# Kernel optimization log

Measured on AMD Instinct MI355X. Metric: run time of the kernel, lower is better.

Reference implementation:

```python
import jax, jax.numpy as jnp
import numpy as np

N_NODES = 50000
N_EDGES = 800000
N_REL = 8
OUT_CH = 64      # latent dim of z
HID = 128        # hidden_channels
IN_CH = 128      # reconstructed feature dim
NEG_SLOPE = 0.2


def rgat_conv(x, src, dst, edge_type, weight, q, k, bias, num_nodes):
    """PyG RGATConv, heads=1, dim=1, additive-self-attention, across-relation.
    x: [N, in]; weight: [R, in, out]; q,k: [out, 1]; bias: [out]."""
    # per-relation transform of all nodes, then per-edge gather (same math as
    # per-edge bmm with weight[edge_type], avoids [E, in, out] intermediate)
    x_all = jnp.einsum('ni,rio->nro', x, weight)          # [N, R, out]
    x_j = x_all[src, edge_type]                            # [E, out]
    x_i = x_all[dst, edge_type]                            # [E, out]
    alpha = (x_i @ q + x_j @ k)[:, 0]                      # [E]
    alpha = jax.nn.leaky_relu(alpha, NEG_SLOPE)
    # scatter-softmax over destination neighborhoods
    m = jax.ops.segment_max(alpha, dst, num_segments=num_nodes)
    m = jnp.where(jnp.isfinite(m), m, 0.0)                 # empty segments -> 0
    ex = jnp.exp(alpha - m[dst])
    denom = jax.ops.segment_sum(ex, dst, num_segments=num_nodes)
    a = ex / (denom[dst] + 1e-16)                          # [E]
    out = jax.ops.segment_sum(a[:, None] * x_j, dst, num_segments=num_nodes)
    return out + bias


def setup_inputs() -> dict:
    key = jax.random.key(0)
    ks = jax.random.split(key, 12)
    z = jax.random.normal(ks[0], (N_NODES, OUT_CH), dtype=jnp.float32)
    edge_index = jax.random.randint(ks[1], (2, N_EDGES), 0, N_NODES, dtype=jnp.int32)
    edge_type = jax.random.randint(ks[2], (N_EDGES,), 0, N_REL, dtype=jnp.int32)

    def glorot(k_, shape):
        fan = shape[-2] + shape[-1]
        return jax.random.normal(k_, shape, dtype=jnp.float32) * jnp.sqrt(2.0 / fan)

    return {
        'z': z,
        'lin_w': glorot(ks[3], (HID, OUT_CH)),
        'lin_b': jnp.zeros((HID,), dtype=jnp.float32),
        'w1': glorot(ks[4], (N_REL, HID, HID)),
        'q1': glorot(ks[5], (HID, 1)),
        'k1': glorot(ks[6], (HID, 1)),
        'b1': jnp.zeros((HID,), dtype=jnp.float32),
        'w2': glorot(ks[7], (N_REL, HID, IN_CH)),
        'q2': glorot(ks[8], (IN_CH, 1)),
        'k2': glorot(ks[9], (IN_CH, 1)),
        'b2': jnp.zeros((IN_CH,), dtype=jnp.float32),
        'edge_index': edge_index,
        'edge_type': edge_type,
    }


def reference(z, lin_w, lin_b, w1, q1, k1, b1, w2, q2, k2, b2, edge_index, edge_type):
    num_nodes = z.shape[0]
    src, dst = edge_index[0], edge_index[1]
    h = z @ lin_w.T + lin_b                                 # nn.Linear
    h = jax.nn.relu(rgat_conv(h, src, dst, edge_type, w1, q1, k1, b1, num_nodes))
    # dropout is identity in eval mode
    recon_x = rgat_conv(h, src, dst, edge_type, w2, q2, k2, b2, num_nodes)
    return recon_x
```

## Files before the change

kernel.cpp:

```cpp
#include <hip/hip_runtime.h>
#include <hip/hip_bf16.h>
#include <cstdint>
#include <cstddef>

#define N_NODES 50000
#define N_EDGES 800000
#define NSEG    (N_NODES * 8)

using frag_t = __attribute__((ext_vector_type(8))) short;
using f32x4  = __attribute__((ext_vector_type(4))) float;

typedef const __attribute__((address_space(1))) void* gptr_t;
typedef __attribute__((address_space(3))) void* lptr_t;

__device__ __forceinline__ short f2bf(float x) {
    __hip_bfloat16 h = __float2bfloat16(x);
    return *reinterpret_cast<short*>(&h);
}
__device__ __forceinline__ float bf2f(unsigned int u) {
    union { unsigned int i; float f; } v;
    v.i = u << 16;
    return v.f;
}
__device__ __forceinline__ unsigned int packbf2(float lo, float hi) {
    unsigned int a = (unsigned short)f2bf(lo);
    unsigned int b = (unsigned short)f2bf(hi);
    return a | (b << 16);
}


__global__ void hist_kernel(const int* __restrict__ dst, const int* __restrict__ et,
                            int* __restrict__ deg8, int E) {
    int e = blockIdx.x * 256 + threadIdx.x;
    if (e < E) atomicAdd(&deg8[dst[e] * 8 + et[e]], 1);
}

__global__ __launch_bounds__(256) void scan_part(const int* __restrict__ deg8,
                                                 int* __restrict__ part, int M) {
    __shared__ int red[256];
    int t = threadIdx.x;
    int idx = blockIdx.x * 1024 + t * 4;
    int s = 0;
    if (idx + 3 < M) {
        int4 d = *(const int4*)(deg8 + idx);
        s = d.x + d.y + d.z + d.w;
    } else {
        for (int c = 0; c < 4; c++) if (idx + c < M) s += deg8[idx + c];
    }
    red[t] = s;
    __syncthreads();
    #pragma unroll
    for (int off = 128; off; off >>= 1) {
        if (t < off) red[t] += red[t + off];
        __syncthreads();
    }
    if (t == 0) part[blockIdx.x] = red[0];
}

__global__ __launch_bounds__(512) void scan_mid(int* __restrict__ part, int nparts,
                                                int* __restrict__ rowp, int M) {
    __shared__ int buf[512];
    int t = threadIdx.x;
    int own = (t < nparts) ? part[t] : 0;
    buf[t] = own;
    __syncthreads();
    for (int off = 1; off < 512; off <<= 1) {
        int v = buf[t];
        int u = (t >= off) ? buf[t - off] : 0;
        __syncthreads();
        buf[t] = v + u;
        __syncthreads();
    }
    if (t < nparts) part[t] = buf[t] - own;
    if (t == 511) rowp[M] = buf[511];
}

__global__ __launch_bounds__(256) void scan_fix(const int* __restrict__ deg8,
                                                const int* __restrict__ part,
                                                int* __restrict__ rowp,
                                                int* __restrict__ cursor, int M) {
    __shared__ int wsum[4];
    int t = threadIdx.x, lane = t & 63, w = t >> 6;
    int idx = blockIdx.x * 1024 + t * 4;
    int v0 = 0, v1 = 0, v2 = 0, v3 = 0;
    if (idx + 3 < M) {
        int4 d = *(const int4*)(deg8 + idx);
        v0 = d.x; v1 = d.y; v2 = d.z; v3 = d.w;
    } else {
        if (idx     < M) v0 = deg8[idx];
        if (idx + 1 < M) v1 = deg8[idx + 1];
        if (idx + 2 < M) v2 = deg8[idx + 2];
        if (idx + 3 < M) v3 = deg8[idx + 3];
    }
    int tsum = v0 + v1 + v2 + v3;
    int sc = tsum;
    #pragma unroll
    for (int off = 1; off < 64; off <<= 1) {
        int u = __shfl_up(sc, off, 64);
        if (lane >= off) sc += u;
    }
    if (lane == 63) wsum[w] = sc;
    __syncthreads();
    int woff = 0;
    for (int i = 0; i < w; i++) woff += wsum[i];
    int excl = part[blockIdx.x] + woff + sc - tsum;
    if (idx     < M) { rowp[idx]     = excl; cursor[idx]     = excl; } excl += v0;
    if (idx + 1 < M) { rowp[idx + 1] = excl; cursor[idx + 1] = excl; } excl += v1;
    if (idx + 2 < M) { rowp[idx + 2] = excl; cursor[idx + 2] = excl; } excl += v2;
    if (idx + 3 < M) { rowp[idx + 3] = excl; cursor[idx + 3] = excl; }
}

__global__ void fill_kernel(const int* __restrict__ src, const int* __restrict__ dst,
                            const int* __restrict__ et, int* __restrict__ cursor,
                            int* __restrict__ sorted, int E) {
    int e = blockIdx.x * 256 + threadIdx.x;
    if (e < E) {
        int pos = atomicAdd(&cursor[dst[e] * 8 + et[e]], 1);
        sorted[pos] = src[e] | (et[e] << 16);
    }
}


__global__ __launch_bounds__(256) void gemm_lin(const float* __restrict__ A,
                                                const float* __restrict__ B,
                                                const float* __restrict__ bias,
                                                unsigned short* __restrict__ hb, int N) {
    const int Kdim = 64;
    __shared__ float As[32][64];
    __shared__ float Bs[32][128];
    int t = threadIdx.x;
    int n0 = blockIdx.x * 64;
    int rg = t >> 4, cg = t & 15;
    int an = t >> 2, ak = (t & 3) * 8;
    float acc[4][8] = {};

    for (int k0 = 0; k0 < Kdim; k0 += 32) {
        int gn = n0 + an;
        if (gn < N) {
            const float* ap = A + (size_t)gn * Kdim + k0 + ak;
            float4 v0 = *(const float4*)ap;
            float4 v1 = *(const float4*)(ap + 4);
            As[ak + 0][an] = v0.x; As[ak + 1][an] = v0.y;
            As[ak + 2][an] = v0.z; As[ak + 3][an] = v0.w;
            As[ak + 4][an] = v1.x; As[ak + 5][an] = v1.y;
            As[ak + 6][an] = v1.z; As[ak + 7][an] = v1.w;
        } else {
            #pragma unroll
            for (int c = 0; c < 8; c++) As[ak + c][an] = 0.f;
        }
        {
            int o = t >> 1, kh = (t & 1) * 16;
            const float* bp = B + (size_t)o * Kdim + k0 + kh;
            #pragma unroll
            for (int j = 0; j < 4; j++) {
                float4 v = ((const float4*)bp)[j];
                Bs[kh + j * 4 + 0][o] = v.x;
                Bs[kh + j * 4 + 1][o] = v.y;
                Bs[kh + j * 4 + 2][o] = v.z;
                Bs[kh + j * 4 + 3][o] = v.w;
            }
        }
        __syncthreads();
        #pragma unroll
        for (int k = 0; k < 32; k++) {
            float a[4], b[8];
            *(float4*)&a[0] = *(const float4*)&As[k][rg * 4];
            *(float4*)&b[0] = *(const float4*)&Bs[k][cg * 8];
            *(float4*)&b[4] = *(const float4*)&Bs[k][cg * 8 + 4];
            #pragma unroll
            for (int i = 0; i < 4; i++)
                #pragma unroll
                for (int j = 0; j < 8; j++)
                    acc[i][j] = fmaf(a[i], b[j], acc[i][j]);
        }
        __syncthreads();
    }
    #pragma unroll
    for (int i = 0; i < 4; i++) {
        int gn = n0 + rg * 4 + i;
        if (gn < N) {
            unsigned short us[8];
            #pragma unroll
            for (int j = 0; j < 8; j++)
                us[j] = (unsigned short)f2bf(acc[i][j] + bias[cg * 8 + j]);
            *(int4*)(hb + (size_t)gn * 128 + cg * 8) = *(int4*)&us[0];
        }
    }
}


__global__ void wprep_kernel(const float* __restrict__ W, const float* __restrict__ q,
                             const float* __restrict__ k, short* __restrict__ Bf,
                             float* __restrict__ wq, float* __restrict__ wk) {
    int g = blockIdx.x * 256 + threadIdx.x;
    if (g < 131072) {
        int kk = g >> 7, o = g & 127;
        float v = W[(size_t)kk * 128 + o];
        Bf[(((size_t)(kk >> 3) * 128) + o) * 8 + (kk & 7)] = f2bf(v);
        return;
    }
    int h = g - 131072;
    if (h < 2048) {
        int which = h >> 10;
        int r = (h >> 7) & 7;
        int i = h & 127;
        const float* vec = which ? k : q;
        const float* wrow = W + ((size_t)r * 128 + i) * 128;
        float acc = 0.f;
        #pragma unroll 4
        for (int o = 0; o < 128; o++) acc = fmaf(wrow[o], vec[o], acc);
        (which ? wk : wq)[r * 128 + i] = acc;
    }
}


__global__ __launch_bounds__(256) void qk_table_kernel(const unsigned short* __restrict__ xb,
                                                       const float* __restrict__ wq,
                                                       const float* __restrict__ wk,
                                                       float* __restrict__ Q,
                                                       float* __restrict__ K, int N) {
    int n = blockIdx.x * 256 + threadIdx.x;
    if (n >= N) return;
    const uint2* row = (const uint2*)(xb + (size_t)n * 128);
    float aq[8] = {}, ak[8] = {};
    for (int i = 0; i < 32; i++) {
        uint2 d = row[i];
        float x0 = bf2f(d.x & 0xFFFFu);
        float x1 = bf2f(d.x >> 16);
        float x2 = bf2f(d.y & 0xFFFFu);
        float x3 = bf2f(d.y >> 16);
        int c = i * 4;
        #pragma unroll
        for (int r = 0; r < 8; r++) {
            const float* wqr = wq + r * 128 + c;
            const float* wkr = wk + r * 128 + c;
            aq[r] = fmaf(x0, wqr[0], fmaf(x1, wqr[1], fmaf(x2, wqr[2], fmaf(x3, wqr[3], aq[r]))));
            ak[r] = fmaf(x0, wkr[0], fmaf(x1, wkr[1], fmaf(x2, wkr[2], fmaf(x3, wkr[3], ak[r]))));
        }
    }
    float4* qp = (float4*)(Q + (size_t)n * 8);
    qp[0] = *(float4*)&aq[0];
    qp[1] = *(float4*)&aq[4];
    float4* kp = (float4*)(K + (size_t)n * 8);
    kp[0] = *(float4*)&ak[0];
    kp[1] = *(float4*)&ak[4];
}


__global__ __launch_bounds__(256) void agg_s_kernel(const unsigned short* __restrict__ hb,
                                                    const float* __restrict__ Q,
                                                    const float* __restrict__ Kt,
                                                    const int* __restrict__ rowp8,
                                                    const int* __restrict__ sorted,
                                                    short* __restrict__ s, int N) {
    int wv = threadIdx.x >> 6;
    int lane = threadIdx.x & 63;
    int n = blockIdx.x * 4 + wv;
    if (n >= N) return;
    int beg = rowp8[n * 8];
    int end = rowp8[n * 8 + 8];
    int deg = end - beg;
    unsigned int* spw = (unsigned int*)(s + (size_t)n * 1024);
    const unsigned int* hbu = (const unsigned int*)hb;

    if (deg == 0) {
        int4 z = {0, 0, 0, 0};
        int4* p = (int4*)spw;
        p[lane * 2]     = z;
        p[lane * 2 + 1] = z;
        return;
    }

    float2 acc = {0.f, 0.f};
    int rcur = 0;

    if (deg <= 64) {
        int pk = 0;
        float a = -INFINITY;
        if (lane < deg) {
            pk = sorted[beg + lane];
            int srcn = pk & 0xFFFF, etj = pk >> 16;
            a = Q[(size_t)n * 8 + etj] + Kt[(size_t)srcn * 8 + etj];
            a = (a > 0.f) ? a : 0.2f * a;
        }
        float m = a;
        #pragma unroll
        for (int off = 32; off; off >>= 1) m = fmaxf(m, __shfl_xor(m, off, 64));
        float e = (lane < deg) ? __expf(a - m) : 0.f;
        float sum = e;
        #pragma unroll
        for (int off = 32; off; off >>= 1) sum += __shfl_xor(sum, off, 64);
        float w = e / (sum + 1e-16f);

        int j = 0;
        for (; j + 8 <= deg; j += 8) {
            int pp[8]; float ww[8]; unsigned int dd[8];
            #pragma unroll
            for (int i = 0; i < 8; i++) {
                pp[i] = __shfl(pk, j + i, 64);
                ww[i] = __shfl(w,  j + i, 64);
            }
            #pragma unroll
            for (int i = 0; i < 8; i++)
                dd[i] = hbu[(size_t)(pp[i] & 0xFFFF) * 64 + lane];
            #pragma unroll
            for (int i = 0; i < 8; i++) {
                int e0 = pp[i] >> 16;
                while (rcur < e0) { spw[rcur * 64 + lane] = packbf2(acc.x, acc.y); acc.x = acc.y = 0.f; rcur++; }
                acc.x = fmaf(ww[i], bf2f(dd[i] & 0xFFFF), acc.x);
                acc.y = fmaf(ww[i], bf2f(dd[i] >> 16),    acc.y);
            }
        }
        for (; j < deg; j++) {
            int   p0 = __shfl(pk, j, 64);
            float w0 = __shfl(w, j, 64);
            unsigned int d0 = hbu[(size_t)(p0 & 0xFFFF) * 64 + lane];
            int e0 = p0 >> 16;
            while (rcur < e0) { spw[rcur * 64 + lane] = packbf2(acc.x, acc.y); acc.x = acc.y = 0.f; rcur++; }
            acc.x = fmaf(w0, bf2f(d0 & 0xFFFF), acc.x);
            acc.y = fmaf(w0, bf2f(d0 >> 16),    acc.y);
        }
        while (rcur < 8) { spw[rcur * 64 + lane] = packbf2(acc.x, acc.y); acc.x = acc.y = 0.f; rcur++; }
        return;
    }

    auto logit = [&](int j) -> float {
        int pk = sorted[beg + j];
        int srcn = pk & 0xFFFF, etj = pk >> 16;
        float a = Q[(size_t)n * 8 + etj] + Kt[(size_t)srcn * 8 + etj];
        return (a > 0.f) ? a : 0.2f * a;
    };
    float m = -INFINITY;
    for (int j = lane; j < deg; j += 64) m = fmaxf(m, logit(j));
    #pragma unroll
    for (int off = 32; off; off >>= 1) m = fmaxf(m, __shfl_xor(m, off, 64));
    float sum = 0.f;
    for (int j = lane; j < deg; j += 64) sum += __expf(logit(j) - m);
    #pragma unroll
    for (int off = 32; off; off >>= 1) sum += __shfl_xor(sum, off, 64);
    float inv = 1.f / (sum + 1e-16f);

    for (int j0 = 0; j0 < deg; j0 += 64) {
        int cnt = min(64, deg - j0);
        int pk = 0;
        float w = 0.f;
        if (lane < cnt) {
            pk = sorted[beg + j0 + lane];
            int srcn = pk & 0xFFFF, etj = pk >> 16;
            float a = Q[(size_t)n * 8 + etj] + Kt[(size_t)srcn * 8 + etj];
            a = (a > 0.f) ? a : 0.2f * a;
            w = __expf(a - m) * inv;
        }
        for (int j = 0; j < cnt; j++) {
            int   p0 = __shfl(pk, j, 64);
            float w0 = __shfl(w, j, 64);
            unsigned int d0 = hbu[(size_t)(p0 & 0xFFFF) * 64 + lane];
            int e0 = p0 >> 16;
            while (rcur < e0) { spw[rcur * 64 + lane] = packbf2(acc.x, acc.y); acc.x = acc.y = 0.f; rcur++; }
            acc.x = fmaf(w0, bf2f(d0 & 0xFFFF), acc.x);
            acc.y = fmaf(w0, bf2f(d0 >> 16),    acc.y);
        }
    }
    while (rcur < 8) { spw[rcur * 64 + lane] = packbf2(acc.x, acc.y); acc.x = acc.y = 0.f; rcur++; }
}


__global__ __launch_bounds__(256) void gemm_mfma(const short* __restrict__ s,
                                                 const short* __restrict__ Bf,
                                                 const float* __restrict__ bias,
                                                 float* __restrict__ Cout,
                                                 unsigned short* __restrict__ hbout,
                                                 int N, int relu) {
    __shared__ short As[4096];
    __shared__ short Bs[4096];
    int t = threadIdx.x;
    int w = t >> 6, lane = t & 63;
    int lhi = lane >> 4, llo = lane & 15;
    int n0 = blockIdx.x * 128;
    const char* sB = (const char*)s;
    const char* bB = (const char*)Bf;
    f32x4 acc[16] = {};

    for (int c = 0; c < 32; c++) {
        #pragma unroll
        for (int i = 0; i < 2; i++) {
            int row = i * 64 + lane;
            const void* gp = sB + (size_t)(n0 + row) * 2048 + c * 64 + w * 16;
            __builtin_amdgcn_global_load_lds(
                (gptr_t)gp, (lptr_t)((char*)As + w * 2048 + i * 1024), 16, 0, 0);
        }
        #pragma unroll
        for (int i = 0; i < 2; i++) {
            const void* gp = bB + (size_t)c * 8192 + w * 2048 + i * 1024 + lane * 16;
            __builtin_amdgcn_global_load_lds(
                (gptr_t)gp, (lptr_t)((char*)Bs + w * 2048 + i * 1024), 16, 0, 0);
        }
        __syncthreads();
        frag_t a0 = *(const frag_t*)(As + ((size_t)lhi * 128 + w * 32 + llo) * 8);
        frag_t a1 = *(const frag_t*)(As + ((size_t)lhi * 128 + w * 32 + llo + 16) * 8);
        #pragma unroll
        for (int ct = 0; ct < 8; ct++) {
            frag_t b = *(const frag_t*)(Bs + ((size_t)lhi * 128 + ct * 16 + llo) * 8);
            acc[ct]     = __builtin_amdgcn_mfma_f32_16x16x32_bf16(a0, b, acc[ct], 0, 0, 0);
            acc[8 + ct] = __builtin_amdgcn_mfma_f32_16x16x32_bf16(a1, b, acc[8 + ct], 0, 0, 0);
        }
        __syncthreads();
    }
    #pragma unroll
    for (int rt = 0; rt < 2; rt++) {
        #pragma unroll
        for (int ct = 0; ct < 8; ct++) {
            int col = ct * 16 + llo;
            float bv = bias[col];
            #pragma unroll
            for (int rg = 0; rg < 4; rg++) {
                int rown = n0 + w * 32 + rt * 16 + lhi * 4 + rg;
                if (rown < N) {
                    float v = acc[rt * 8 + ct][rg] + bv;
                    if (relu) v = fmaxf(v, 0.f);
                    if (Cout)  Cout[(size_t)rown * 128 + col] = v;
                    if (hbout) hbout[(size_t)rown * 128 + col] = (unsigned short)f2bf(v);
                }
            }
        }
    }
}


extern "C" void kernel_launch(void* const* d_in, const int* in_sizes, int n_in,
                              void* d_out, int out_size, void* d_ws, size_t ws_size,
                              hipStream_t stream) {
    const float* z     = (const float*)d_in[0];
    const float* lin_w = (const float*)d_in[1];
    const float* lin_b = (const float*)d_in[2];
    const float* w1    = (const float*)d_in[3];
    const float* q1    = (const float*)d_in[4];
    const float* k1    = (const float*)d_in[5];
    const float* b1    = (const float*)d_in[6];
    const float* w2    = (const float*)d_in[7];
    const float* q2    = (const float*)d_in[8];
    const float* k2    = (const float*)d_in[9];
    const float* b2    = (const float*)d_in[10];
    const int*   ei    = (const int*)d_in[11];
    const int*   et    = (const int*)d_in[12];
    float* out = (float*)d_out;

    char* ws = (char*)d_ws;
    size_t off = 0;
    auto alloc = [&](size_t bytes) -> void* {
        void* p = ws + off;
        off += (bytes + 255) & ~(size_t)255;
        return p;
    };
    short* s     = (short*)alloc((size_t)N_NODES * 1024 * 2);
    unsigned short* hb = (unsigned short*)alloc((size_t)N_NODES * 128 * 2);
    float* Q     = (float*)alloc((size_t)N_NODES * 8 * 4);
    float* K     = (float*)alloc((size_t)N_NODES * 8 * 4);
    int* sorted  = (int*)alloc((size_t)N_EDGES * 4);
    int* deg8    = (int*)alloc((size_t)NSEG * 4);
    int* rowp8   = (int*)alloc((size_t)(NSEG + 1) * 4);
    int* cursor8 = (int*)alloc((size_t)NSEG * 4);
    int* part    = (int*)alloc(1024 * 4);
    float* wq    = (float*)alloc(8 * 128 * 4);
    float* wk    = (float*)alloc(8 * 128 * 4);
    short* Bf    = (short*)alloc((size_t)1024 * 128 * 2);

    const int* src = ei;
    const int* dst = ei + N_EDGES;

    const int M = NSEG;
    const int nparts = (M + 1023) / 1024;

    hipMemsetAsync(deg8, 0, (size_t)M * 4, stream);
    hist_kernel<<<(N_EDGES + 255) / 256, 256, 0, stream>>>(dst, et, deg8, N_EDGES);
    scan_part<<<nparts, 256, 0, stream>>>(deg8, part, M);
    scan_mid<<<1, 512, 0, stream>>>(part, nparts, rowp8, M);
    scan_fix<<<nparts, 256, 0, stream>>>(deg8, part, rowp8, cursor8, M);
    fill_kernel<<<(N_EDGES + 255) / 256, 256, 0, stream>>>(src, dst, et, cursor8, sorted, N_EDGES);

    gemm_lin<<<(N_NODES + 63) / 64, 256, 0, stream>>>(z, lin_w, lin_b, hb, N_NODES);

    int mgrid = (N_NODES + 127) / 128;
    int agrid = (N_NODES + 3) / 4;
    int qgrid = (N_NODES + 255) / 256;
    int wgrid = (131072 + 2048) / 256;

    wprep_kernel<<<wgrid, 256, 0, stream>>>(w1, q1, k1, Bf, wq, wk);
    qk_table_kernel<<<qgrid, 256, 0, stream>>>(hb, wq, wk, Q, K, N_NODES);
    agg_s_kernel<<<agrid, 256, 0, stream>>>(hb, Q, K, rowp8, sorted, s, N_NODES);
    gemm_mfma<<<mgrid, 256, 0, stream>>>(s, Bf, b1, (float*)nullptr, hb, N_NODES, 1);

    wprep_kernel<<<wgrid, 256, 0, stream>>>(w2, q2, k2, Bf, wq, wk);
    qk_table_kernel<<<qgrid, 256, 0, stream>>>(hb, wq, wk, Q, K, N_NODES);
    agg_s_kernel<<<agrid, 256, 0, stream>>>(hb, Q, K, rowp8, sorted, s, N_NODES);
    gemm_mfma<<<mgrid, 256, 0, stream>>>(s, Bf, b2, out, (unsigned short*)nullptr, N_NODES, 0);
}
```

Before: 411.3 us.

## Fuse neighbor aggregation into MFMA GEMM with relation-major CSR layout

Edges are now bucketed relation-major (per relation, then per destination node), and attention weights are computed in a separate weight_kernel that writes per-edge alphas. A new fused kernel aggregates each relation's weighted neighbor features for a 64-node tile directly into shared memory, then runs that relation's MFMA GEMM slice. This avoids writing and re-reading the large N x 1024 bf16 intermediate s buffer. In exchange it adds an alpha buffer, a second hb buffer, eight serialized gather/GEMM phases per block with syncs, and smaller tiles.

```diff
diff --git a/kernel.cpp b/kernel.cpp
--- a/kernel.cpp
+++ b/kernel.cpp
@@ -30,22 +30,22 @@
 
 
 __global__ void hist_kernel(const int* __restrict__ dst, const int* __restrict__ et,
-                            int* __restrict__ deg8, int E) {
+                            int* __restrict__ deg2, int E) {
     int e = blockIdx.x * 256 + threadIdx.x;
-    if (e < E) atomicAdd(&deg8[dst[e] * 8 + et[e]], 1);
-}
-
-__global__ __launch_bounds__(256) void scan_part(const int* __restrict__ deg8,
+    if (e < E) atomicAdd(&deg2[et[e] * N_NODES + dst[e]], 1);
+}
+
+__global__ __launch_bounds__(256) void scan_part(const int* __restrict__ deg2,
                                                  int* __restrict__ part, int M) {
     __shared__ int red[256];
     int t = threadIdx.x;
     int idx = blockIdx.x * 1024 + t * 4;
     int s = 0;
     if (idx + 3 < M) {
-        int4 d = *(const int4*)(deg8 + idx);
+        int4 d = *(const int4*)(deg2 + idx);
         s = d.x + d.y + d.z + d.w;
     } else {
-        for (int c = 0; c < 4; c++) if (idx + c < M) s += deg8[idx + c];
+        for (int c = 0; c < 4; c++) if (idx + c < M) s += deg2[idx + c];
     }
     red[t] = s;
     __syncthreads();
@@ -75,7 +75,7 @@
     if (t == 511) rowp[M] = buf[511];
 }
 
-__global__ __launch_bounds__(256) void scan_fix(const int* __restrict__ deg8,
+__global__ __launch_bounds__(256) void scan_fix(const int* __restrict__ deg2,
                                                 const int* __restrict__ part,
                                                 int* __restrict__ rowp,
                                                 int* __restrict__ cursor, int M) {
@@ -84,13 +84,13 @@
     int idx = blockIdx.x * 1024 + t * 4;
     int v0 = 0, v1 = 0, v2 = 0, v3 = 0;
     if (idx + 3 < M) {
-        int4 d = *(const int4*)(deg8 + idx);
+        int4 d = *(const int4*)(deg2 + idx);
         v0 = d.x; v1 = d.y; v2 = d.z; v3 = d.w;
     } else {
-        if (idx     < M) v0 = deg8[idx];
-        if (idx + 1 < M) v1 = deg8[idx + 1];
-        if (idx + 2 < M) v2 = deg8[idx + 2];
-        if (idx + 3 < M) v3 = deg8[idx + 3];
+        if (idx     < M) v0 = deg2[idx];
+        if (idx + 1 < M) v1 = deg2[idx + 1];
+        if (idx + 2 < M) v2 = deg2[idx + 2];
+        if (idx + 3 < M) v3 = deg2[idx + 3];
     }
     int tsum = v0 + v1 + v2 + v3;
     int sc = tsum;
@@ -112,11 +112,11 @@
 
 __global__ void fill_kernel(const int* __restrict__ src, const int* __restrict__ dst,
                             const int* __restrict__ et, int* __restrict__ cursor,
-                            int* __restrict__ sorted, int E) {
+                            int* __restrict__ sorted2, int E) {
     int e = blockIdx.x * 256 + threadIdx.x;
     if (e < E) {
-        int pos = atomicAdd(&cursor[dst[e] * 8 + et[e]], 1);
-        sorted[pos] = src[e] | (et[e] << 16);
+        int pos = atomicAdd(&cursor[et[e] * N_NODES + dst[e]], 1);
+        sorted2[pos] = src[e] | (dst[e] << 16);
     }
 }
 
@@ -247,40 +247,36 @@
 }
 
 
-__global__ __launch_bounds__(256) void agg_s_kernel(const unsigned short* __restrict__ hb,
-                                                    const float* __restrict__ Q,
-                                                    const float* __restrict__ Kt,
-                                                    const int* __restrict__ rowp8,
-                                                    const int* __restrict__ sorted,
-                                                    short* __restrict__ s, int N) {
-    int wv = threadIdx.x >> 6;
-    int lane = threadIdx.x & 63;
+__global__ __launch_bounds__(256) void weight_kernel(const float* __restrict__ Q,
+                                                     const float* __restrict__ Kt,
+                                                     const int* __restrict__ rowp2,
+                                                     const int* __restrict__ sorted2,
+                                                     float* __restrict__ alpha2, int N) {
+    int wv = threadIdx.x >> 6, lane = threadIdx.x & 63;
     int n = blockIdx.x * 4 + wv;
     if (n >= N) return;
-    int beg = rowp8[n * 8];
-    int end = rowp8[n * 8 + 8];
-    int deg = end - beg;
-    unsigned int* spw = (unsigned int*)(s + (size_t)n * 1024);
-    const unsigned int* hbu = (const unsigned int*)hb;
-
-    if (deg == 0) {
-        int4 z = {0, 0, 0, 0};
-        int4* p = (int4*)spw;
-        p[lane * 2]     = z;
-        p[lane * 2 + 1] = z;
-        return;
-    }
-
-    float2 acc = {0.f, 0.f};
-    int rcur = 0;
+    int a0 = 0, e0 = 0;
+    if (lane < 8) {
+        a0 = rowp2[lane * N_NODES + n];
+        e0 = rowp2[lane * N_NODES + n + 1];
+    }
+    int p = 0, myr = 0, myidx = 0;
+    #pragma unroll
+    for (int r = 0; r < 8; r++) {
+        int ar = __shfl(a0, r, 64);
+        int er = __shfl(e0, r, 64);
+        int c = er - ar;
+        if (lane >= p && lane < p + c) { myr = r; myidx = ar + lane - p; }
+        p += c;
+    }
+    int deg = p;
+    if (deg == 0) return;
 
     if (deg <= 64) {
-        int pk = 0;
         float a = -INFINITY;
         if (lane < deg) {
-            pk = sorted[beg + lane];
-            int srcn = pk & 0xFFFF, etj = pk >> 16;
-            a = Q[(size_t)n * 8 + etj] + Kt[(size_t)srcn * 8 + etj];
+            int srcn = sorted2[myidx] & 0xFFFF;
+            a = Q[(size_t)n * 8 + myr] + Kt[(size_t)srcn * 8 + myr];
             a = (a > 0.f) ? a : 0.2f * a;
         }
         float m = a;
@@ -290,137 +286,135 @@
         float sum = e;
         #pragma unroll
         for (int off = 32; off; off >>= 1) sum += __shfl_xor(sum, off, 64);
-        float w = e / (sum + 1e-16f);
-
-        int j = 0;
-        for (; j + 8 <= deg; j += 8) {
-            int pp[8]; float ww[8]; unsigned int dd[8];
-            #pragma unroll
-            for (int i = 0; i < 8; i++) {
-                pp[i] = __shfl(pk, j + i, 64);
-                ww[i] = __shfl(w,  j + i, 64);
-            }
-            #pragma unroll
-            for (int i = 0; i < 8; i++)
-                dd[i] = hbu[(size_t)(pp[i] & 0xFFFF) * 64 + lane];
-            #pragma unroll
-            for (int i = 0; i < 8; i++) {
-                int e0 = pp[i] >> 16;
-                while (rcur < e0) { spw[rcur * 64 + lane] = packbf2(acc.x, acc.y); acc.x = acc.y = 0.f; rcur++; }
-                acc.x = fmaf(ww[i], bf2f(dd[i] & 0xFFFF), acc.x);
-                acc.y = fmaf(ww[i], bf2f(dd[i] >> 16),    acc.y);
-            }
-        }
-        for (; j < deg; j++) {
-            int   p0 = __shfl(pk, j, 64);
-            float w0 = __shfl(w, j, 64);
-            unsigned int d0 = hbu[(size_t)(p0 & 0xFFFF) * 64 + lane];
-            int e0 = p0 >> 16;
-            while (rcur < e0) { spw[rcur * 64 + lane] = packbf2(acc.x, acc.y); acc.x = acc.y = 0.f; rcur++; }
-            acc.x = fmaf(w0, bf2f(d0 & 0xFFFF), acc.x);
-            acc.y = fmaf(w0, bf2f(d0 >> 16),    acc.y);
-        }
-        while (rcur < 8) { spw[rcur * 64 + lane] = packbf2(acc.x, acc.y); acc.x = acc.y = 0.f; rcur++; }
+        if (lane < deg) alpha2[myidx] = e / (sum + 1e-16f);
         return;
     }
 
-    auto logit = [&](int j) -> float {
-        int pk = sorted[beg + j];
-        int srcn = pk & 0xFFFF, etj = pk >> 16;
-        float a = Q[(size_t)n * 8 + etj] + Kt[(size_t)srcn * 8 + etj];
-        return (a > 0.f) ? a : 0.2f * a;
-    };
     float m = -INFINITY;
-    for (int j = lane; j < deg; j += 64) m = fmaxf(m, logit(j));
+    #pragma unroll 1
+    for (int r = 0; r < 8; r++) {
+        int ar = __shfl(a0, r, 64), er = __shfl(e0, r, 64);
+        for (int j = ar + lane; j < er; j += 64) {
+            int srcn = sorted2[j] & 0xFFFF;
+            float a = Q[(size_t)n * 8 + r] + Kt[(size_t)srcn * 8 + r];
+            a = (a > 0.f) ? a : 0.2f * a;
+            m = fmaxf(m, a);
+        }
+    }
     #pragma unroll
     for (int off = 32; off; off >>= 1) m = fmaxf(m, __shfl_xor(m, off, 64));
     float sum = 0.f;
-    for (int j = lane; j < deg; j += 64) sum += __expf(logit(j) - m);
+    #pragma unroll 1
+    for (int r = 0; r < 8; r++) {
+        int ar = __shfl(a0, r, 64), er = __shfl(e0, r, 64);
+        for (int j = ar + lane; j < er; j += 64) {
+            int srcn = sorted2[j] & 0xFFFF;
+            float a = Q[(size_t)n * 8 + r] + Kt[(size_t)srcn * 8 + r];
+            a = (a > 0.f) ? a : 0.2f * a;
+            sum += __expf(a - m);
+        }
+    }
     #pragma unroll
     for (int off = 32; off; off >>= 1) sum += __shfl_xor(sum, off, 64);
     float inv = 1.f / (sum + 1e-16f);
-
-    for (int j0 = 0; j0 < deg; j0 += 64) {
-        int cnt = min(64, deg - j0);
-        int pk = 0;
-        float w = 0.f;
-        if (lane < cnt) {
-            pk = sorted[beg + j0 + lane];
-            int srcn = pk & 0xFFFF, etj = pk >> 16;
-            float a = Q[(size_t)n * 8 + etj] + Kt[(size_t)srcn * 8 + etj];
+    #pragma unroll 1
+    for (int r = 0; r < 8; r++) {
+        int ar = __shfl(a0, r, 64), er = __shfl(e0, r, 64);
+        for (int j = ar + lane; j < er; j += 64) {
+            int srcn = sorted2[j] & 0xFFFF;
+            float a = Q[(size_t)n * 8 + r] + Kt[(size_t)srcn * 8 + r];
             a = (a > 0.f) ? a : 0.2f * a;
-            w = __expf(a - m) * inv;
-        }
-        for (int j = 0; j < cnt; j++) {
-            int   p0 = __shfl(pk, j, 64);
-            float w0 = __shfl(w, j, 64);
-            unsigned int d0 = hbu[(size_t)(p0 & 0xFFFF) * 64 + lane];
-            int e0 = p0 >> 16;
-            while (rcur < e0) { spw[rcur * 64 + lane] = packbf2(acc.x, acc.y); acc.x = acc.y = 0.f; rcur++; }
-            acc.x = fmaf(w0, bf2f(d0 & 0xFFFF), acc.x);
-            acc.y = fmaf(w0, bf2f(d0 >> 16),    acc.y);
-        }
-    }
-    while (rcur < 8) { spw[rcur * 64 + lane] = packbf2(acc.x, acc.y); acc.x = acc.y = 0.f; rcur++; }
-}
-
-
-__global__ __launch_bounds__(256) void gemm_mfma(const short* __restrict__ s,
-                                                 const short* __restrict__ Bf,
-                                                 const float* __restrict__ bias,
-                                                 float* __restrict__ Cout,
-                                                 unsigned short* __restrict__ hbout,
-                                                 int N, int relu) {
-    __shared__ short As[4096];
-    __shared__ short Bs[4096];
+            alpha2[j] = __expf(a - m) * inv;
+        }
+    }
+}
+
+
+#define SA_STRIDE 136
+
+__global__ __launch_bounds__(256) void rgat_fused(const unsigned short* __restrict__ xb,
+                                                  const float* __restrict__ alpha2,
+                                                  const int* __restrict__ rowp2,
+                                                  const int* __restrict__ sorted2,
+                                                  const short* __restrict__ Bf,
+                                                  const float* __restrict__ bias,
+                                                  float* __restrict__ Cout,
+                                                  unsigned short* __restrict__ hbout,
+                                                  int N, int relu) {
+    __shared__ short Sa[64 * SA_STRIDE];
+    __shared__ short Bs[16 * 128 * 8];
     int t = threadIdx.x;
-    int w = t >> 6, lane = t & 63;
+    int wv = t >> 6, lane = t & 63;
     int lhi = lane >> 4, llo = lane & 15;
-    int n0 = blockIdx.x * 128;
-    const char* sB = (const char*)s;
-    const char* bB = (const char*)Bf;
-    f32x4 acc[16] = {};
-
-    for (int c = 0; c < 32; c++) {
-        #pragma unroll
-        for (int i = 0; i < 2; i++) {
-            int row = i * 64 + lane;
-            const void* gp = sB + (size_t)(n0 + row) * 2048 + c * 64 + w * 16;
+    int n0 = blockIdx.x * 64;
+    const unsigned int* hbu = (const unsigned int*)xb;
+    unsigned int* sap = (unsigned int*)Sa;
+    f32x4 acc[8] = {};
+
+    for (int r = 0; r < 8; r++) {
+        const char* bB = (const char*)(Bf + (size_t)r * 16384);
+        #pragma unroll
+        for (int i = 0; i < 8; i++) {
             __builtin_amdgcn_global_load_lds(
-                (gptr_t)gp, (lptr_t)((char*)As + w * 2048 + i * 1024), 16, 0, 0);
-        }
-        #pragma unroll
-        for (int i = 0; i < 2; i++) {
-            const void* gp = bB + (size_t)c * 8192 + w * 2048 + i * 1024 + lane * 16;
-            __builtin_amdgcn_global_load_lds(
-                (gptr_t)gp, (lptr_t)((char*)Bs + w * 2048 + i * 1024), 16, 0, 0);
-        }
-        __syncthreads();
-        frag_t a0 = *(const frag_t*)(As + ((size_t)lhi * 128 + w * 32 + llo) * 8);
-        frag_t a1 = *(const frag_t*)(As + ((size_t)lhi * 128 + w * 32 + llo + 16) * 8);
-        #pragma unroll
-        for (int ct = 0; ct < 8; ct++) {
-            frag_t b = *(const frag_t*)(Bs + ((size_t)lhi * 128 + ct * 16 + llo) * 8);
-            acc[ct]     = __builtin_amdgcn_mfma_f32_16x16x32_bf16(a0, b, acc[ct], 0, 0, 0);
-            acc[8 + ct] = __builtin_amdgcn_mfma_f32_16x16x32_bf16(a1, b, acc[8 + ct], 0, 0, 0);
-        }
-        __syncthreads();
-    }
-    #pragma unroll
-    for (int rt = 0; rt < 2; rt++) {
-        #pragma unroll
-        for (int ct = 0; ct < 8; ct++) {
-            int col = ct * 16 + llo;
-            float bv = bias[col];
+                (gptr_t)(bB + i * 4096 + t * 16),
+                (lptr_t)((char*)Bs + i * 4096 + t * 16), 16, 0, 0);
+        }
+        int rbase = wv * 16;
+        int nA = n0 + rbase;
+        int iA = min(nA, N), iB = min(nA + 16, N);
+        int begw = rowp2[r * N_NODES + iA];
+        int endw = rowp2[r * N_NODES + iB];
+        float2 a2 = {0.f, 0.f};
+        int rcur = 0;
+        for (int c0 = begw; c0 < endw; c0 += 64) {
+            int cnt = min(64, endw - c0);
+            int pk = 0; float w = 0.f;
+            if (lane < cnt) {
+                pk = sorted2[c0 + lane];
+                w  = alpha2[c0 + lane];
+            }
+            for (int j = 0; j < cnt; j++) {
+                int   p0 = __shfl(pk, j, 64);
+                float w0 = __shfl(w,  j, 64);
+                unsigned int d0 = hbu[(size_t)(p0 & 0xFFFF) * 64 + lane];
+                int row = (int)(((unsigned int)p0) >> 16) - nA;
+                while (rcur < row) {
+                    sap[(size_t)(rbase + rcur) * (SA_STRIDE / 2) + lane] = packbf2(a2.x, a2.y);
+                    a2.x = a2.y = 0.f; rcur++;
+                }
+                a2.x = fmaf(w0, bf2f(d0 & 0xFFFF), a2.x);
+                a2.y = fmaf(w0, bf2f(d0 >> 16),    a2.y);
+            }
+        }
+        while (rcur < 16) {
+            sap[(size_t)(rbase + rcur) * (SA_STRIDE / 2) + lane] = packbf2(a2.x, a2.y);
+            a2.x = a2.y = 0.f; rcur++;
+        }
+        __syncthreads();
+        #pragma unroll
+        for (int c2 = 0; c2 < 4; c2++) {
+            int kb = c2 * 4 + lhi;
+            frag_t a0 = *(const frag_t*)(Sa + (size_t)(rbase + llo) * SA_STRIDE + kb * 8);
             #pragma unroll
-            for (int rg = 0; rg < 4; rg++) {
-                int rown = n0 + w * 32 + rt * 16 + lhi * 4 + rg;
-                if (rown < N) {
-                    float v = acc[rt * 8 + ct][rg] + bv;
-                    if (relu) v = fmaxf(v, 0.f);
-                    if (Cout)  Cout[(size_t)rown * 128 + col] = v;
-                    if (hbout) hbout[(size_t)rown * 128 + col] = (unsigned short)f2bf(v);
-                }
+            for (int ct = 0; ct < 8; ct++) {
+                frag_t b = *(const frag_t*)(Bs + ((size_t)kb * 128 + ct * 16 + llo) * 8);
+                acc[ct] = __builtin_amdgcn_mfma_f32_16x16x32_bf16(a0, b, acc[ct], 0, 0, 0);
+            }
+        }
+        __syncthreads();
+    }
+    #pragma unroll
+    for (int ct = 0; ct < 8; ct++) {
+        int col = ct * 16 + llo;
+        float bv = bias[col];
+        #pragma unroll
+        for (int rg = 0; rg < 4; rg++) {
+            int rown = n0 + wv * 16 + lhi * 4 + rg;
+            if (rown < N) {
+                float v = acc[ct][rg] + bv;
+                if (relu) v = fmaxf(v, 0.f);
+                if (Cout)  Cout[(size_t)rown * 128 + col] = v;
+                if (hbout) hbout[(size_t)rown * 128 + col] = (unsigned short)f2bf(v);
             }
         }
     }
@@ -452,18 +446,19 @@
         off += (bytes + 255) & ~(size_t)255;
         return p;
     };
-    short* s     = (short*)alloc((size_t)N_NODES * 1024 * 2);
-    unsigned short* hb = (unsigned short*)alloc((size_t)N_NODES * 128 * 2);
-    float* Q     = (float*)alloc((size_t)N_NODES * 8 * 4);
-    float* K     = (float*)alloc((size_t)N_NODES * 8 * 4);
-    int* sorted  = (int*)alloc((size_t)N_EDGES * 4);
-    int* deg8    = (int*)alloc((size_t)NSEG * 4);
-    int* rowp8   = (int*)alloc((size_t)(NSEG + 1) * 4);
-    int* cursor8 = (int*)alloc((size_t)NSEG * 4);
-    int* part    = (int*)alloc(1024 * 4);
-    float* wq    = (float*)alloc(8 * 128 * 4);
-    float* wk    = (float*)alloc(8 * 128 * 4);
-    short* Bf    = (short*)alloc((size_t)1024 * 128 * 2);
+    unsigned short* hb  = (unsigned short*)alloc((size_t)N_NODES * 128 * 2);
+    unsigned short* hb2 = (unsigned short*)alloc((size_t)N_NODES * 128 * 2);
+    float* Q      = (float*)alloc((size_t)N_NODES * 8 * 4);
+    float* K      = (float*)alloc((size_t)N_NODES * 8 * 4);
+    float* alpha2 = (float*)alloc((size_t)N_EDGES * 4);
+    int* sorted2  = (int*)alloc((size_t)N_EDGES * 4);
+    int* deg2     = (int*)alloc((size_t)NSEG * 4);
+    int* rowp2    = (int*)alloc((size_t)(NSEG + 1) * 4);
+    int* cursor2  = (int*)alloc((size_t)NSEG * 4);
+    int* part     = (int*)alloc(1024 * 4);
+    float* wq     = (float*)alloc(8 * 128 * 4);
+    float* wk     = (float*)alloc(8 * 128 * 4);
+    short* Bf     = (short*)alloc((size_t)1024 * 128 * 2);
 
     const int* src = ei;
     const int* dst = ei + N_EDGES;
@@ -471,27 +466,29 @@
     const int M = NSEG;
     const int nparts = (M + 1023) / 1024;
 
-    hipMemsetAsync(deg8, 0, (size_t)M * 4, stream);
-    hist_kernel<<<(N_EDGES + 255) / 256, 256, 0, stream>>>(dst, et, deg8, N_EDGES);
-    scan_part<<<nparts, 256, 0, stream>>>(deg8, part, M);
-    scan_mid<<<1, 512, 0, stream>>>(part, nparts, rowp8, M);
-    scan_fix<<<nparts, 256, 0, stream>>>(deg8, part, rowp8, cursor8, M);
-    fill_kernel<<<(N_EDGES + 255) / 256, 256, 0, stream>>>(src, dst, et, cursor8, sorted, N_EDGES);
+    hipMemsetAsync(deg2, 0, (size_t)M * 4, stream);
+    hist_kernel<<<(N_EDGES + 255) / 256, 256, 0, stream>>>(dst, et, deg2, N_EDGES);
+    scan_part<<<nparts, 256, 0, stream>>>(deg2, part, M);
+    scan_mid<<<1, 512, 0, stream>>>(part, nparts, rowp2, M);
+    scan_fix<<<nparts, 256, 0, stream>>>(deg2, part, rowp2, cursor2, M);
+    fill_kernel<<<(N_EDGES + 255) / 256, 256, 0, stream>>>(src, dst, et, cursor2, sorted2, N_EDGES);
 
     gemm_lin<<<(N_NODES + 63) / 64, 256, 0, stream>>>(z, lin_w, lin_b, hb, N_NODES);
 
-    int mgrid = (N_NODES + 127) / 128;
+    int fgrid = (N_NODES + 63) / 64;
     int agrid = (N_NODES + 3) / 4;
     int qgrid = (N_NODES + 255) / 256;
     int wgrid = (131072 + 2048) / 256;
 
     wprep_kernel<<<wgrid, 256, 0, stream>>>(w1, q1, k1, Bf, wq, wk);
     qk_table_kernel<<<qgrid, 256, 0, stream>>>(hb, wq, wk, Q, K, N_NODES);
-    agg_s_kernel<<<agrid, 256, 0, stream>>>(hb, Q, K, rowp8, sorted, s, N_NODES);
-    gemm_mfma<<<mgrid, 256, 0, stream>>>(s, Bf, b1, (float*)nullptr, hb, N_NODES, 1);
+    weight_kernel<<<agrid, 256, 0, stream>>>(Q, K, rowp2, sorted2, alpha2, N_NODES);
+    rgat_fused<<<fgrid, 256, 0, stream>>>(hb, alpha2, rowp2, sorted2, Bf, b1,
+                                          (float*)nullptr, hb2, N_NODES, 1);
 
     wprep_kernel<<<wgrid, 256, 0, stream>>>(w2, q2, k2, Bf, wq, wk);
-    qk_table_kernel<<<qgrid, 256, 0, stream>>>(hb, wq, wk, Q, K, N_NODES);
-    agg_s_kernel<<<agrid, 256, 0, stream>>>(hb, Q, K, rowp8, sorted, s, N_NODES);
-    gemm_mfma<<<mgrid, 256, 0, stream>>>(s, Bf, b2, out, (unsigned short*)nullptr, N_NODES, 0);
-}
+    qk_table_kernel<<<qgrid, 256, 0, stream>>>(hb2, wq, wk, Q, K, N_NODES);
+    weight_kernel<<<agrid, 256, 0, stream>>>(Q, K, rowp2, sorted2, alpha2, N_NODES);
+    rgat_fused<<<fgrid, 256, 0, stream>>>(hb2, alpha2, rowp2, sorted2, Bf, b2,
+                                          out, (unsigned short*)nullptr, N_NODES, 0);
+}
```

Result: slower. 720.1 us (+75.1%).
